# Performance work log

Measured on AMD Instinct MI355X. Metric: run time of the kernel, lower is better.

## Reference

```python
import jax, jax.numpy as jnp
import numpy as np

K = 4          # non-zeros kept per block
BLOCK = 8      # block size along last dim (block_dim = -1)


def _block_topk_mask(score):
    # score last dim is a multiple of BLOCK; block_dim == -1 so no transpose needed.
    s = score.reshape(-1, BLOCK)                       # [n_blocks, BLOCK]
    # argsort ascending; drop the (BLOCK-K) smallest entries per block
    idx = jnp.argsort(s, axis=1)[:, : BLOCK - K]       # [n_blocks, BLOCK-K]
    rows = jnp.arange(s.shape[0])[:, None]
    mask = jnp.ones_like(s).at[rows, idx].set(0.0)     # scatter zeros at pruned idx
    return mask.reshape(score.shape)


def setup_inputs() -> dict:
    key = jax.random.key(0)
    k1, k2 = jax.random.split(key)
    x = jax.random.normal(k1, (8192, 8192), dtype=jnp.float32)
    score = jax.random.normal(k2, (8192, 8192), dtype=jnp.float32)  # learned score param
    return {"x": x, "score": score}


def reference(x, score):
    # Sparsify.forward (training, BlockTopK): mask = sparseness.get_mask(score); out = x * mask
    mask = _block_topk_mask(score)
    return x * mask
```

## Files before the change

kernel.cpp:

```cpp
#include <hip/hip_runtime.h>


typedef float v4f __attribute__((ext_vector_type(4)));

__device__ __forceinline__ v4f topk_half_block(v4f sv, v4f xv, bool odd) {
    float s[4] = {sv.x, sv.y, sv.z, sv.w};
    float x[4] = {xv.x, xv.y, xv.z, xv.w};

    float t[4];
#pragma unroll
    for (int k = 0; k < 4; ++k)
        t[k] = __shfl_xor(s[k], 1);

    v4f o;
#pragma unroll
    for (int k = 0; k < 4; ++k) {
        int rank = 0;
#pragma unroll
        for (int j = 0; j < 4; ++j) {
            if (j != k)
                rank += (s[j] < s[k]) || ((s[j] == s[k]) && (j < k));
            rank += (t[j] < s[k]) || ((t[j] == s[k]) && odd);
        }
        o[k] = (rank >= 4) ? x[k] : 0.0f;
    }
    return o;
}

__global__ __launch_bounds__(256) void sparsify_topk_kernel(
    const v4f* __restrict__ x4,
    const v4f* __restrict__ s4,
    v4f* __restrict__ o4,
    int n4)
{
    const bool odd = (threadIdx.x & 1) != 0;
    const int stride = gridDim.x * blockDim.x;

    int i = blockIdx.x * blockDim.x + threadIdx.x;

    for (; i + stride < n4; i += 2 * stride) {
        const int i0 = i;
        const int i1 = i + stride;

        v4f sv0 = s4[i0];
        v4f sv1 = s4[i1];
        v4f xv0 = __builtin_nontemporal_load(&x4[i0]);
        v4f xv1 = __builtin_nontemporal_load(&x4[i1]);

        v4f r0 = topk_half_block(sv0, xv0, odd);
        v4f r1 = topk_half_block(sv1, xv1, odd);

        __builtin_nontemporal_store(r0, &o4[i0]);
        __builtin_nontemporal_store(r1, &o4[i1]);
    }
    if (i < n4) {
        v4f sv = s4[i];
        v4f xv = __builtin_nontemporal_load(&x4[i]);
        v4f r  = topk_half_block(sv, xv, odd);
        __builtin_nontemporal_store(r, &o4[i]);
    }
}

extern "C" void kernel_launch(void* const* d_in, const int* in_sizes, int n_in,
                              void* d_out, int out_size, void* d_ws, size_t ws_size,
                              hipStream_t stream) {
    const v4f* x4 = (const v4f*)d_in[0];
    const v4f* s4 = (const v4f*)d_in[1];
    v4f* o4 = (v4f*)d_out;

    int n = in_sizes[0];
    int n4 = n / 4;

    const int threads = 256;
    int grid = 2048;
    sparsify_topk_kernel<<<grid, threads, 0, stream>>>(x4, s4, o4, n4);
}
```

Baseline: 609.5 us.

## Replace grid-stride loop with one-shot grid of 4-chunk blocks, drop nontemporal hints

Swaps the fixed 2048-block grid-stride loop for a grid sized to cover the data exactly, with each block handling four contiguous 256-element chunks. All loads for a thread are issued before any compute, which raises memory-level parallelism. The nontemporal load and store builtins are replaced by plain accesses. The grid becomes about 16K blocks, which adds block-launch overhead in exchange for removing loop control and the dependence between iterations.

```diff
diff --git a/kernel.cpp b/kernel.cpp
--- a/kernel.cpp
+++ b/kernel.cpp
@@ -27,6 +27,8 @@
     return o;
 }
 
+#define CHUNKS 4
+
 __global__ __launch_bounds__(256) void sparsify_topk_kernel(
     const v4f* __restrict__ x4,
     const v4f* __restrict__ s4,
@@ -34,30 +36,30 @@
     int n4)
 {
     const bool odd = (threadIdx.x & 1) != 0;
-    const int stride = gridDim.x * blockDim.x;
+    const int base = blockIdx.x * (256 * CHUNKS) + threadIdx.x;
 
-    int i = blockIdx.x * blockDim.x + threadIdx.x;
+    if (base + 3 * 256 < n4) {
+        v4f sv[CHUNKS], xv[CHUNKS];
+#pragma unroll
+        for (int c = 0; c < CHUNKS; ++c) sv[c] = s4[base + c * 256];
+#pragma unroll
+        for (int c = 0; c < CHUNKS; ++c) xv[c] = x4[base + c * 256];
 
-    for (; i + stride < n4; i += 2 * stride) {
-        const int i0 = i;
-        const int i1 = i + stride;
+        v4f r[CHUNKS];
+#pragma unroll
+        for (int c = 0; c < CHUNKS; ++c) r[c] = topk_half_block(sv[c], xv[c], odd);
 
-        v4f sv0 = s4[i0];
-        v4f sv1 = s4[i1];
-        v4f xv0 = __builtin_nontemporal_load(&x4[i0]);
-        v4f xv1 = __builtin_nontemporal_load(&x4[i1]);
-
-        v4f r0 = topk_half_block(sv0, xv0, odd);
-        v4f r1 = topk_half_block(sv1, xv1, odd);
-
-        __builtin_nontemporal_store(r0, &o4[i0]);
-        __builtin_nontemporal_store(r1, &o4[i1]);
-    }
-    if (i < n4) {
-        v4f sv = s4[i];
-        v4f xv = __builtin_nontemporal_load(&x4[i]);
-        v4f r  = topk_half_block(sv, xv, odd);
-        __builtin_nontemporal_store(r, &o4[i]);
+#pragma unroll
+        for (int c = 0; c < CHUNKS; ++c) o4[base + c * 256] = r[c];
+    } else {
+#pragma unroll
+        for (int c = 0; c < CHUNKS; ++c) {
+            int i = base + c * 256;
+            if (i < n4) {
+                v4f rv = topk_half_block(s4[i], x4[i], odd);
+                o4[i] = rv;
+            }
+        }
     }
 }
 
@@ -72,6 +74,7 @@
     int n4 = n / 4;
 
     const int threads = 256;
-    int grid = 2048;
+    const int per_block = threads * CHUNKS;
+    int grid = (n4 + per_block - 1) / per_block;
     sparsify_topk_kernel<<<grid, threads, 0, stream>>>(x4, s4, o4, n4);
 }
```

Measured after the change: 576.7 us. -5.4%, faster.
